# Optimization experiments

Hardware: AMD Instinct MI355X
Metric: run time of the kernel (lower is better)

## Reference

```python
import jax, jax.numpy as jnp
import numpy as np

B, S, D, H = 4, 2048, 768, 12
HD = D // H  # head_dim = 64


def setup_inputs() -> dict:
    key = jax.random.key(0)
    ks = jax.random.split(key, 5)
    scale = 0.02
    return {
        "x": jax.random.normal(ks[0], (B, S, D), dtype=jnp.float32),
        "wq": jax.random.normal(ks[1], (D, D), dtype=jnp.float32) * scale,
        "wk": jax.random.normal(ks[2], (D, D), dtype=jnp.float32) * scale,
        "wv": jax.random.normal(ks[3], (D, D), dtype=jnp.float32) * scale,
        "wo": jax.random.normal(ks[4], (D, D), dtype=jnp.float32) * scale,
        "bo": jnp.zeros((D,), dtype=jnp.float32),
    }


def reference(x, wq, wk, wv, wo, bo):
    b, s, d = x.shape
    # torch Linear: y = x @ W.T ; qkv_bias=False
    q = (x @ wq.T).reshape(b, s, H, HD).transpose(0, 2, 1, 3)  # [b,h,s,hd]
    k = (x @ wk.T).reshape(b, s, H, HD).transpose(0, 2, 1, 3)
    v = (x @ wv.T).reshape(b, s, H, HD).transpose(0, 2, 1, 3)
    scores = jnp.einsum("bhqd,bhkd->bhqk", q, k)  # full [b,h,s,s] score matrix
    causal = jnp.triu(jnp.ones((s, s), dtype=bool), k=1)
    scores = jnp.where(causal, -jnp.inf, scores)
    attn = jax.nn.softmax(scores / jnp.sqrt(jnp.float32(HD)), axis=-1)
    ctx = jnp.einsum("bhqk,bhkd->bhqd", attn, v)
    ctx = ctx.transpose(0, 2, 1, 3).reshape(b, s, d)
    return ctx @ wo.T + bo  # dropout is identity in eval mode
```

## Files before the change

### kernel.cpp

```cpp
#include <hip/hip_runtime.h>

#define H 12
#define S 2048
#define D 768
#define HD 64
#define BATCH 4
#define M_TOT (BATCH * S)

typedef __attribute__((ext_vector_type(8))) short bf16x8;
typedef __attribute__((ext_vector_type(4))) float f32x4;

__device__ __forceinline__ ushort f2bf(float f) {
  unsigned int x = __float_as_uint(f);
  x += 0x7fffu + ((x >> 16) & 1u);
  return (ushort)(x >> 16);
}

__device__ __forceinline__ uint cvt_pk_bf16(float lo, float hi) {
  uint r;
  asm("v_cvt_pk_bf16_f32 %0, %1, %2" : "=v"(r) : "v"(lo), "v"(hi));
  return r;
}

__device__ __forceinline__ void gload_lds16(const void* gsrc, void* lds) {
  __builtin_amdgcn_global_load_lds(
      (const __attribute__((address_space(1))) unsigned int*)gsrc,
      (__attribute__((address_space(3))) unsigned int*)lds, 16, 0, 0);
}

__global__ __launch_bounds__(256) void cast_all(
    const float* __restrict__ x, const float* __restrict__ wq,
    const float* __restrict__ wk, const float* __restrict__ wv,
    const float* __restrict__ wo, ushort* __restrict__ xb,
    ushort* __restrict__ wqb, ushort* __restrict__ wkb,
    ushort* __restrict__ wvb, ushort* __restrict__ wob) {
  const int NX = M_TOT * D / 4;
  const int NW = D * D / 4;
  int i = blockIdx.x * 256 + threadIdx.x;
  const float* src; ushort* dst; int off;
  if (i < NX) { src = x; dst = xb; off = i; }
  else {
    int j = i - NX; int w = j / NW; off = j - w * NW;
    src = (w == 0) ? wq : (w == 1) ? wk : (w == 2) ? wv : wo;
    dst = (w == 0) ? wqb : (w == 1) ? wkb : (w == 2) ? wvb : wob;
  }
  float4 f = reinterpret_cast<const float4*>(src)[off];
  ushort4 u;
  u.x = f2bf(f.x); u.y = f2bf(f.y); u.z = f2bf(f.z); u.w = f2bf(f.w);
  reinterpret_cast<ushort4*>(dst)[off] = u;
}

__global__ __launch_bounds__(256) void gemm_qkv(
    const ushort* __restrict__ xb, const ushort* __restrict__ wqb,
    const ushort* __restrict__ wkb, const ushort* __restrict__ wvb,
    ushort* __restrict__ qb, ushort* __restrict__ kb_,
    ushort* __restrict__ vtb, float qscale) {
  __shared__ ushort SM[3][6144];
  const int tid = threadIdx.x;
  const int lane = tid & 63, wid = tid >> 6;
  const int g = lane >> 4, li = lane & 15;
  const int wm = wid >> 1, wn = wid & 1;

  const int wg = blockIdx.x;
  const int which = wg / 768, r = wg - which * 768;
  const ushort *Ap, *Wp; ushort* ob; float osc; int m0, n0; bool vt;
  if (which < 2) {
    vt = false;
    m0 = (r & 127) * 64;
    n0 = (r >> 7) * 128;
    Ap = xb;
    if (which == 0) { Wp = wqb; ob = qb; osc = qscale; }
    else            { Wp = wkb; ob = kb_; osc = 1.0f; }
  } else {
    vt = true;
    m0 = (r % 12) * 64;
    n0 = (r / 12) * 128;
    Ap = wvb; Wp = xb; ob = vtb; osc = 1.0f;
  }

  const int rsub = lane >> 2;
  const int coff = (((lane & 3) ^ ((rsub >> 1) & 3)) << 3);

  auto stage = [&](int buf, int k0) {
    gload_lds16(&Ap[(size_t)(m0 + wid * 16 + rsub) * 768 + k0 + coff],
                &SM[buf][wid * 16 * 32]);
#pragma unroll
    for (int rnd = 0; rnd < 2; ++rnd) {
      const int row0 = rnd * 64 + wid * 16;
      gload_lds16(&Wp[(size_t)(n0 + row0 + rsub) * 768 + k0 + coff],
                  &SM[buf][2048 + row0 * 32]);
    }
  };

  f32x4 acc[2][4] = {};
  stage(0, 0);
  stage(1, 32);

  int cur = 0, pre = 2;
  for (int kt = 0; kt < 24; ++kt) {
    if (kt < 23) asm volatile("s_waitcnt vmcnt(3) lgkmcnt(0)" ::: "memory");
    else         asm volatile("s_waitcnt vmcnt(0) lgkmcnt(0)" ::: "memory");
    __builtin_amdgcn_s_barrier();
    if (kt + 2 < 24) stage(pre, (kt + 2) * 32);

    bf16x8 a[2], b[4];
#pragma unroll
    for (int i = 0; i < 2; ++i) {
      const int row = wm * 32 + i * 16 + li;
      a[i] = *reinterpret_cast<const bf16x8*>(
          &SM[cur][row * 32 + ((g ^ ((row >> 1) & 3)) << 3)]);
    }
#pragma unroll
    for (int j = 0; j < 4; ++j) {
      const int row = wn * 64 + j * 16 + li;
      b[j] = *reinterpret_cast<const bf16x8*>(
          &SM[cur][2048 + row * 32 + ((g ^ ((row >> 1) & 3)) << 3)]);
    }
    __builtin_amdgcn_s_setprio(1);
#pragma unroll
    for (int i = 0; i < 2; ++i)
#pragma unroll
      for (int j = 0; j < 4; ++j)
        acc[i][j] = __builtin_amdgcn_mfma_f32_16x16x32_bf16(a[i], b[j], acc[i][j], 0, 0, 0);
    __builtin_amdgcn_s_setprio(0);

    cur = (cur == 2) ? 0 : cur + 1;
    pre = (pre == 2) ? 0 : pre + 1;
  }

  __syncthreads();
  ushort* Cs = &SM[0][0];
#pragma unroll
  for (int i = 0; i < 2; ++i)
#pragma unroll
    for (int j = 0; j < 4; ++j)
#pragma unroll
      for (int rr = 0; rr < 4; ++rr) {
        const int row = wm * 32 + i * 16 + g * 4 + rr;
        const int col = wn * 64 + j * 16 + li;
        const int pc = ((((col >> 3) ^ (row & 7)) << 3) | (col & 7));
        Cs[row * 128 + pc] = f2bf(acc[i][j][rr] * osc);
      }
  __syncthreads();

  const int row = tid >> 2, q4 = tid & 3;
  ushort* dst;
  if (!vt) {
    const int m = m0 + row;
    const int b_ = m >> 11, s_ = m & 2047;
    const int h_ = (n0 >> 6) + (q4 >> 1);
    dst = &ob[(((size_t)b_ * H + h_) * S + s_) * HD + (q4 & 1) * 32];
  } else {
    const int mf = m0 + row;
    const int b_ = n0 >> 11;
    const int h_ = mf >> 6, hd_ = mf & 63;
    dst = &ob[(((size_t)b_ * H + h_) * HD + hd_) * S + (n0 & 2047) + q4 * 32];
  }
#pragma unroll
  for (int c8 = 0; c8 < 4; ++c8) {
    const int col = q4 * 32 + c8 * 8;
    const int chunk = (col >> 3) ^ (row & 7);
    bf16x8 vv = *reinterpret_cast<const bf16x8*>(&Cs[row * 128 + chunk * 8]);
    *reinterpret_cast<bf16x8*>(&dst[c8 * 8]) = vv;
  }
}

__global__ __launch_bounds__(256) void gemm_wo(const ushort* __restrict__ A,
                                               const ushort* __restrict__ W,
                                               float* __restrict__ out_f,
                                               const float* __restrict__ bias) {
  __shared__ ushort SM[3][6144];
  const int tid = threadIdx.x;
  const int lane = tid & 63, wid = tid >> 6;
  const int g = lane >> 4, li = lane & 15;
  const int wm = wid >> 1, wn = wid & 1;
  const int m0 = blockIdx.x * 64, n0 = blockIdx.y * 128;

  const int rsub = lane >> 2;
  const int coff = (((lane & 3) ^ ((rsub >> 1) & 3)) << 3);

  auto stage = [&](int buf, int k0) {
    gload_lds16(&A[(size_t)(m0 + wid * 16 + rsub) * 768 + k0 + coff],
                &SM[buf][wid * 16 * 32]);
#pragma unroll
    for (int rnd = 0; rnd < 2; ++rnd) {
      const int row0 = rnd * 64 + wid * 16;
      gload_lds16(&W[(size_t)(n0 + row0 + rsub) * 768 + k0 + coff],
                  &SM[buf][2048 + row0 * 32]);
    }
  };

  f32x4 acc[2][4] = {};
  stage(0, 0);
  stage(1, 32);

  int cur = 0, pre = 2;
  for (int kt = 0; kt < 24; ++kt) {
    if (kt < 23) asm volatile("s_waitcnt vmcnt(3) lgkmcnt(0)" ::: "memory");
    else         asm volatile("s_waitcnt vmcnt(0) lgkmcnt(0)" ::: "memory");
    __builtin_amdgcn_s_barrier();
    if (kt + 2 < 24) stage(pre, (kt + 2) * 32);

    bf16x8 a[2], b[4];
#pragma unroll
    for (int i = 0; i < 2; ++i) {
      const int row = wm * 32 + i * 16 + li;
      a[i] = *reinterpret_cast<const bf16x8*>(
          &SM[cur][row * 32 + ((g ^ ((row >> 1) & 3)) << 3)]);
    }
#pragma unroll
    for (int j = 0; j < 4; ++j) {
      const int row = wn * 64 + j * 16 + li;
      b[j] = *reinterpret_cast<const bf16x8*>(
          &SM[cur][2048 + row * 32 + ((g ^ ((row >> 1) & 3)) << 3)]);
    }
    __builtin_amdgcn_s_setprio(1);
#pragma unroll
    for (int i = 0; i < 2; ++i)
#pragma unroll
      for (int j = 0; j < 4; ++j)
        acc[i][j] = __builtin_amdgcn_mfma_f32_16x16x32_bf16(a[i], b[j], acc[i][j], 0, 0, 0);
    __builtin_amdgcn_s_setprio(0);

    cur = (cur == 2) ? 0 : cur + 1;
    pre = (pre == 2) ? 0 : pre + 1;
  }

#pragma unroll
  for (int i = 0; i < 2; ++i)
#pragma unroll
    for (int j = 0; j < 4; ++j)
#pragma unroll
      for (int r = 0; r < 4; ++r) {
        const int m = m0 + wm * 32 + i * 16 + g * 4 + r;
        const int n = n0 + wn * 64 + j * 16 + li;
        out_f[(size_t)m * 768 + n] = acc[i][j][r] + bias[n];
      }
}

__global__ __launch_bounds__(256) void attn_kernel(const ushort* __restrict__ Q,
                                                   const ushort* __restrict__ K,
                                                   const ushort* __restrict__ VT,
                                                   ushort* __restrict__ ctx) {
  __shared__ ushort Ks[2][64 * 64];
  __shared__ ushort Vts[2][64 * 64];
  __shared__ ushort Ps[4][32][72];

  const int tid = threadIdx.x;
  const int lane = tid & 63, wid = tid >> 6;
  const int g = lane >> 4, li = lane & 15;

  const int wg = blockIdx.x;
  const int xcd = wg & 7, t = wg >> 3;
  const int bh = xcd + 8 * (t >> 4);
  const int p = t & 15;
  const int qL = 64 * (31 - p), qS = 64 * p;

  const size_t base = (size_t)bh * S * HD;
  const size_t vtbase = (size_t)bh * HD * S;

  bf16x8 aq[2][2];
#pragma unroll
  for (int f = 0; f < 2; ++f) {
    const size_t qr = base + (size_t)((f ? qS : qL) + wid * 16 + li) * HD;
#pragma unroll
    for (int c = 0; c < 2; ++c)
      aq[f][c] = *reinterpret_cast<const bf16x8*>(&Q[qr + c * 32 + g * 8]);
  }

  f32x4 acc[2][4] = {};
  float lpart[2] = {0.f, 0.f};

  const int nkt = 32 - p;

  const int rsub = lane >> 3;
  const int c8e = (((lane & 7) ^ rsub) << 3);

  auto stage = [&](int buf, int k0) {
#pragma unroll
    for (int rnd = 0; rnd < 2; ++rnd) {
      const int row0 = rnd * 32 + wid * 8;
      gload_lds16(&K[base + (size_t)(k0 + row0 + rsub) * HD + c8e], &Ks[buf][row0 << 6]);
      gload_lds16(&VT[vtbase + (size_t)(row0 + rsub) * S + k0 + c8e], &Vts[buf][row0 << 6]);
    }
  };

  stage(0, 0);

  for (int kt = 0; kt < nkt; ++kt) {
    const int cur = kt & 1;
    const int k0 = kt * 64;
    const bool doS = (kt <= p);

    asm volatile("s_waitcnt vmcnt(0)" ::: "memory");
    __syncthreads();
    if (kt + 1 < nkt) stage(cur ^ 1, k0 + 64);

    f32x4 sc[2][4];
    __builtin_amdgcn_s_setprio(1);
#pragma unroll
    for (int ct = 0; ct < 4; ++ct) {
      const int row = ct * 16 + li, r7 = row & 7;
      const ushort* kr = &Ks[cur][row << 6];
      bf16x8 kb0 = *reinterpret_cast<const bf16x8*>(&kr[(g ^ r7) << 3]);
      bf16x8 kb1 = *reinterpret_cast<const bf16x8*>(&kr[((4 + g) ^ r7) << 3]);
      {
        f32x4 z = {};
        z = __builtin_amdgcn_mfma_f32_16x16x32_bf16(kb0, aq[0][0], z, 0, 0, 0);
        z = __builtin_amdgcn_mfma_f32_16x16x32_bf16(kb1, aq[0][1], z, 0, 0, 0);
        sc[0][ct] = z;
      }
      if (doS) {
        f32x4 z = {};
        z = __builtin_amdgcn_mfma_f32_16x16x32_bf16(kb0, aq[1][0], z, 0, 0, 0);
        z = __builtin_amdgcn_mfma_f32_16x16x32_bf16(kb1, aq[1][1], z, 0, 0, 0);
        sc[1][ct] = z;
      }
    }
    __builtin_amdgcn_s_setprio(0);

    if (kt == nkt - 1) {
      const int q = qL + wid * 16 + li;
#pragma unroll
      for (int ct = 0; ct < 4; ++ct)
#pragma unroll
        for (int r = 0; r < 4; ++r)
          if (k0 + ct * 16 + 4 * g + r > q) sc[0][ct][r] = -1e30f;
    }
    if (kt == p) {
      const int q = qS + wid * 16 + li;
#pragma unroll
      for (int ct = 0; ct < 4; ++ct)
#pragma unroll
        for (int r = 0; r < 4; ++r)
          if (k0 + ct * 16 + 4 * g + r > q) sc[1][ct][r] = -1e30f;
    }

#pragma unroll
    for (int f = 0; f < 2; ++f) {
      if (f == 1 && !doS) break;
#pragma unroll
      for (int ct = 0; ct < 4; ++ct) {
        float p0 = __builtin_amdgcn_exp2f(sc[f][ct][0]);
        float p1 = __builtin_amdgcn_exp2f(sc[f][ct][1]);
        float p2 = __builtin_amdgcn_exp2f(sc[f][ct][2]);
        float p3 = __builtin_amdgcn_exp2f(sc[f][ct][3]);
        lpart[f] += (p0 + p1) + (p2 + p3);
        uint2 pw;
        pw.x = cvt_pk_bf16(p0, p1);
        pw.y = cvt_pk_bf16(p2, p3);
        *reinterpret_cast<uint2*>(&Ps[wid][f * 16 + li][ct * 16 + 4 * g]) = pw;
      }
    }

    bf16x8 pa[2][2];
    pa[0][0] = *reinterpret_cast<const bf16x8*>(&Ps[wid][li][g * 8]);
    pa[0][1] = *reinterpret_cast<const bf16x8*>(&Ps[wid][li][32 + g * 8]);
    if (doS) {
      pa[1][0] = *reinterpret_cast<const bf16x8*>(&Ps[wid][16 + li][g * 8]);
      pa[1][1] = *reinterpret_cast<const bf16x8*>(&Ps[wid][16 + li][32 + g * 8]);
    }
    __builtin_amdgcn_s_setprio(1);
#pragma unroll
    for (int dt = 0; dt < 4; ++dt) {
      const int row = dt * 16 + li, r7 = row & 7;
      const ushort* vr = &Vts[cur][row << 6];
      bf16x8 vb0 = *reinterpret_cast<const bf16x8*>(&vr[(g ^ r7) << 3]);
      bf16x8 vb1 = *reinterpret_cast<const bf16x8*>(&vr[((4 + g) ^ r7) << 3]);
      acc[0][dt] = __builtin_amdgcn_mfma_f32_16x16x32_bf16(pa[0][0], vb0, acc[0][dt], 0, 0, 0);
      acc[0][dt] = __builtin_amdgcn_mfma_f32_16x16x32_bf16(pa[0][1], vb1, acc[0][dt], 0, 0, 0);
      if (doS) {
        acc[1][dt] = __builtin_amdgcn_mfma_f32_16x16x32_bf16(pa[1][0], vb0, acc[1][dt], 0, 0, 0);
        acc[1][dt] = __builtin_amdgcn_mfma_f32_16x16x32_bf16(pa[1][1], vb1, acc[1][dt], 0, 0, 0);
      }
    }
    __builtin_amdgcn_s_setprio(0);
  }

  const int b = bh / H, h = bh % H;
#pragma unroll
  for (int f = 0; f < 2; ++f) {
    float l = lpart[f];
    l += __shfl_xor(l, 16);
    l += __shfl_xor(l, 32);
#pragma unroll
    for (int r = 0; r < 4; ++r) {
      float inv = 1.0f / __shfl(l, 4 * g + r);
      const int s = (f ? qS : qL) + wid * 16 + 4 * g + r;
#pragma unroll
      for (int dt = 0; dt < 4; ++dt)
        ctx[((size_t)(b * S + s)) * D + h * HD + dt * 16 + li] =
            f2bf(acc[f][dt][r] * inv);
    }
  }
}

extern "C" void kernel_launch(void* const* d_in, const int* in_sizes, int n_in,
                              void* d_out, int out_size, void* d_ws, size_t ws_size,
                              hipStream_t stream) {
  (void)in_sizes; (void)n_in; (void)out_size; (void)ws_size;
  const float* x  = (const float*)d_in[0];
  const float* wq = (const float*)d_in[1];
  const float* wk = (const float*)d_in[2];
  const float* wv = (const float*)d_in[3];
  const float* wo = (const float*)d_in[4];
  const float* bo = (const float*)d_in[5];
  float* out = (float*)d_out;

  const size_t xn = (size_t)M_TOT * D;
  const size_t wn = (size_t)D * D;

  ushort* p = (ushort*)d_ws;
  ushort* x_bf  = p; p += xn;
  ushort* wq_bf = p; p += wn;
  ushort* wk_bf = p; p += wn;
  ushort* wv_bf = p; p += wn;
  ushort* wo_bf = p; p += wn;
  ushort* q_bf  = p; p += xn;
  ushort* k_bf  = p; p += xn;
  ushort* vt_bf = p; p += xn;
  ushort* ctx_bf = x_bf;

  cast_all<<<8448, 256, 0, stream>>>(x, wq, wk, wv, wo,
                                     x_bf, wq_bf, wk_bf, wv_bf, wo_bf);

  const float QSCALE = 0.125f * 1.44269504f;
  gemm_qkv<<<2304, 256, 0, stream>>>(x_bf, wq_bf, wk_bf, wv_bf,
                                     q_bf, k_bf, vt_bf, QSCALE);

  attn_kernel<<<768, 256, 0, stream>>>(q_bf, k_bf, vt_bf, ctx_bf);

  gemm_wo<<<dim3(128, 6), 256, 0, stream>>>(ctx_bf, wo_bf, out, bo);
}
```

Baseline: 139.5 us.

## Fuse Q/K/V projections into one tile sharing the x tile

The QKV GEMM now has each workgroup load one 128-row x tile and compute all three projections (Q, K, V) for a 64-wide head slab, so the x tile is staged once instead of three times. V is computed as x·Wv^T and transposed through LDS in the epilogue rather than run as a separate transposed GEMM. The grid shrinks from 2304 to 768 blocks and the pipeline drops from triple to double buffering with a full vmcnt(0) wait, which may expose more load latency. Accumulator registers grow threefold, and launch bounds are set to request 3 blocks per CU.

```diff
diff --git a/kernel.cpp b/kernel.cpp
--- a/kernel.cpp
+++ b/kernel.cpp
@@ -50,118 +50,136 @@
   reinterpret_cast<ushort4*>(dst)[off] = u;
 }
 
-__global__ __launch_bounds__(256) void gemm_qkv(
+__global__ __launch_bounds__(256, 3) void gemm_qkv(
     const ushort* __restrict__ xb, const ushort* __restrict__ wqb,
     const ushort* __restrict__ wkb, const ushort* __restrict__ wvb,
     ushort* __restrict__ qb, ushort* __restrict__ kb_,
     ushort* __restrict__ vtb, float qscale) {
-  __shared__ ushort SM[3][6144];
+  __shared__ ushort SM[2][10240];
   const int tid = threadIdx.x;
   const int lane = tid & 63, wid = tid >> 6;
   const int g = lane >> 4, li = lane & 15;
-  const int wm = wid >> 1, wn = wid & 1;
 
   const int wg = blockIdx.x;
-  const int which = wg / 768, r = wg - which * 768;
-  const ushort *Ap, *Wp; ushort* ob; float osc; int m0, n0; bool vt;
-  if (which < 2) {
-    vt = false;
-    m0 = (r & 127) * 64;
-    n0 = (r >> 7) * 128;
-    Ap = xb;
-    if (which == 0) { Wp = wqb; ob = qb; osc = qscale; }
-    else            { Wp = wkb; ob = kb_; osc = 1.0f; }
-  } else {
-    vt = true;
-    m0 = (r % 12) * 64;
-    n0 = (r / 12) * 128;
-    Ap = wvb; Wp = xb; ob = vtb; osc = 1.0f;
-  }
+  const int mt = wg & 63, slab = wg >> 6;
+  const int m0 = mt * 128, n0 = slab * 64;
+
+  const ushort* xm = xb + (size_t)m0 * 768;
+  const ushort* wqn = wqb + (size_t)n0 * 768;
+  const ushort* wkn = wkb + (size_t)n0 * 768;
+  const ushort* wvn = wvb + (size_t)n0 * 768;
 
   const int rsub = lane >> 2;
   const int coff = (((lane & 3) ^ ((rsub >> 1) & 3)) << 3);
+  const int wrow = wid * 16;
 
   auto stage = [&](int buf, int k0) {
-    gload_lds16(&Ap[(size_t)(m0 + wid * 16 + rsub) * 768 + k0 + coff],
-                &SM[buf][wid * 16 * 32]);
 #pragma unroll
     for (int rnd = 0; rnd < 2; ++rnd) {
-      const int row0 = rnd * 64 + wid * 16;
-      gload_lds16(&Wp[(size_t)(n0 + row0 + rsub) * 768 + k0 + coff],
-                  &SM[buf][2048 + row0 * 32]);
-    }
+      const int row0 = rnd * 64 + wrow;
+      gload_lds16(&xm[(size_t)(row0 + rsub) * 768 + k0 + coff], &SM[buf][row0 * 32]);
+    }
+    gload_lds16(&wqn[(size_t)(wrow + rsub) * 768 + k0 + coff], &SM[buf][4096 + wrow * 32]);
+    gload_lds16(&wkn[(size_t)(wrow + rsub) * 768 + k0 + coff], &SM[buf][6144 + wrow * 32]);
+    gload_lds16(&wvn[(size_t)(wrow + rsub) * 768 + k0 + coff], &SM[buf][8192 + wrow * 32]);
   };
 
-  f32x4 acc[2][4] = {};
+  f32x4 acc[3][2][4] = {};
   stage(0, 0);
-  stage(1, 32);
-
-  int cur = 0, pre = 2;
+
   for (int kt = 0; kt < 24; ++kt) {
-    if (kt < 23) asm volatile("s_waitcnt vmcnt(3) lgkmcnt(0)" ::: "memory");
-    else         asm volatile("s_waitcnt vmcnt(0) lgkmcnt(0)" ::: "memory");
-    __builtin_amdgcn_s_barrier();
-    if (kt + 2 < 24) stage(pre, (kt + 2) * 32);
-
-    bf16x8 a[2], b[4];
+    const int cur = kt & 1;
+    asm volatile("s_waitcnt vmcnt(0)" ::: "memory");
+    __syncthreads();
+    if (kt + 1 < 24) stage(cur ^ 1, (kt + 1) * 32);
+
+    const ushort* bp = &SM[cur][0];
+    bf16x8 a[2];
 #pragma unroll
     for (int i = 0; i < 2; ++i) {
-      const int row = wm * 32 + i * 16 + li;
+      const int row = wid * 32 + i * 16 + li;
       a[i] = *reinterpret_cast<const bf16x8*>(
-          &SM[cur][row * 32 + ((g ^ ((row >> 1) & 3)) << 3)]);
-    }
-#pragma unroll
-    for (int j = 0; j < 4; ++j) {
-      const int row = wn * 64 + j * 16 + li;
-      b[j] = *reinterpret_cast<const bf16x8*>(
-          &SM[cur][2048 + row * 32 + ((g ^ ((row >> 1) & 3)) << 3)]);
-    }
-    __builtin_amdgcn_s_setprio(1);
+          &bp[row * 32 + ((g ^ ((row >> 1) & 3)) << 3)]);
+    }
+#pragma unroll
+    for (int o = 0; o < 3; ++o) {
+      const int off = 4096 + o * 2048;
+      bf16x8 b[4];
+#pragma unroll
+      for (int j = 0; j < 4; ++j) {
+        const int row = j * 16 + li;
+        b[j] = *reinterpret_cast<const bf16x8*>(
+            &bp[off + row * 32 + ((g ^ ((row >> 1) & 3)) << 3)]);
+      }
+      __builtin_amdgcn_s_setprio(1);
+#pragma unroll
+      for (int i = 0; i < 2; ++i)
+#pragma unroll
+        for (int j = 0; j < 4; ++j)
+          acc[o][i][j] = __builtin_amdgcn_mfma_f32_16x16x32_bf16(a[i], b[j], acc[o][i][j], 0, 0, 0);
+      __builtin_amdgcn_s_setprio(0);
+    }
+  }
+
+  ushort* Cs = &SM[0][0];
+  const int b0 = m0 >> 11, sb = m0 & 2047;
+
+  __syncthreads();
+#pragma unroll
+  for (int o = 0; o < 2; ++o)
 #pragma unroll
     for (int i = 0; i < 2; ++i)
 #pragma unroll
       for (int j = 0; j < 4; ++j)
-        acc[i][j] = __builtin_amdgcn_mfma_f32_16x16x32_bf16(a[i], b[j], acc[i][j], 0, 0, 0);
-    __builtin_amdgcn_s_setprio(0);
-
-    cur = (cur == 2) ? 0 : cur + 1;
-    pre = (pre == 2) ? 0 : pre + 1;
-  }
-
+#pragma unroll
+        for (int rr = 0; rr < 4; ++rr) {
+          const int row = wid * 32 + i * 16 + g * 4 + rr;
+          const int col = j * 16 + li;
+          const int pc = ((((col >> 3) ^ (row & 7)) << 3) | (col & 7));
+          const float v = acc[o][i][j][rr] * (o == 0 ? qscale : 1.0f);
+          Cs[o * 8192 + row * 64 + pc] = f2bf(v);
+        }
   __syncthreads();
-  ushort* Cs = &SM[0][0];
+  {
+    const int row = tid >> 1, half = tid & 1;
+    const int m = m0 + row;
+    const size_t rb = (((size_t)b0 * H + slab) * S + (m & 2047)) * HD + half * 32;
+    ushort* dq = &qb[rb];
+    ushort* dk = &kb_[rb];
+#pragma unroll
+    for (int c8 = 0; c8 < 4; ++c8) {
+      const int col = half * 32 + c8 * 8;
+      const int chunk = (col >> 3) ^ (row & 7);
+      *reinterpret_cast<bf16x8*>(&dq[c8 * 8]) =
+          *reinterpret_cast<const bf16x8*>(&Cs[row * 64 + chunk * 8]);
+      *reinterpret_cast<bf16x8*>(&dk[c8 * 8]) =
+          *reinterpret_cast<const bf16x8*>(&Cs[8192 + row * 64 + chunk * 8]);
+    }
+  }
+
+  __syncthreads();
 #pragma unroll
   for (int i = 0; i < 2; ++i)
 #pragma unroll
     for (int j = 0; j < 4; ++j)
 #pragma unroll
       for (int rr = 0; rr < 4; ++rr) {
-        const int row = wm * 32 + i * 16 + g * 4 + rr;
-        const int col = wn * 64 + j * 16 + li;
-        const int pc = ((((col >> 3) ^ (row & 7)) << 3) | (col & 7));
-        Cs[row * 128 + pc] = f2bf(acc[i][j][rr] * osc);
+        const int tok = wid * 32 + i * 16 + g * 4 + rr;
+        const int feat = j * 16 + li;
+        const int pc = ((((tok >> 3) ^ (feat & 7)) << 3) | (tok & 7));
+        Cs[feat * 128 + pc] = f2bf(acc[2][i][j][rr]);
       }
   __syncthreads();
-
-  const int row = tid >> 2, q4 = tid & 3;
-  ushort* dst;
-  if (!vt) {
-    const int m = m0 + row;
-    const int b_ = m >> 11, s_ = m & 2047;
-    const int h_ = (n0 >> 6) + (q4 >> 1);
-    dst = &ob[(((size_t)b_ * H + h_) * S + s_) * HD + (q4 & 1) * 32];
-  } else {
-    const int mf = m0 + row;
-    const int b_ = n0 >> 11;
-    const int h_ = mf >> 6, hd_ = mf & 63;
-    dst = &ob[(((size_t)b_ * H + h_) * HD + hd_) * S + (n0 & 2047) + q4 * 32];
-  }
-#pragma unroll
-  for (int c8 = 0; c8 < 4; ++c8) {
-    const int col = q4 * 32 + c8 * 8;
-    const int chunk = (col >> 3) ^ (row & 7);
-    bf16x8 vv = *reinterpret_cast<const bf16x8*>(&Cs[row * 128 + chunk * 8]);
-    *reinterpret_cast<bf16x8*>(&dst[c8 * 8]) = vv;
+  {
+    const int feat = tid >> 2, qtr = tid & 3;
+    ushort* dv = &vtb[(((size_t)b0 * H + slab) * HD + feat) * S + sb + qtr * 32];
+#pragma unroll
+    for (int c8 = 0; c8 < 4; ++c8) {
+      const int tok = qtr * 32 + c8 * 8;
+      const int chunk = (tok >> 3) ^ (feat & 7);
+      *reinterpret_cast<bf16x8*>(&dv[c8 * 8]) =
+          *reinterpret_cast<const bf16x8*>(&Cs[feat * 128 + chunk * 8]);
+    }
   }
 }
 
@@ -425,8 +443,8 @@
                                      x_bf, wq_bf, wk_bf, wv_bf, wo_bf);
 
   const float QSCALE = 0.125f * 1.44269504f;
-  gemm_qkv<<<2304, 256, 0, stream>>>(x_bf, wq_bf, wk_bf, wv_bf,
-                                     q_bf, k_bf, vt_bf, QSCALE);
+  gemm_qkv<<<768, 256, 0, stream>>>(x_bf, wq_bf, wk_bf, wv_bf,
+                                    q_bf, k_bf, vt_bf, QSCALE);
 
   attn_kernel<<<768, 256, 0, stream>>>(q_bf, k_bf, vt_bf, ctx_bf);
 
```

New measurement: 126.5 us (median of 2 runs). 1.1x faster.
